# Performance work log

Measured on AMD Instinct MI355X. Metric: run time of the kernel, lower is better.

The kernel has to match this reference:

```python
import jax, jax.numpy as jnp
import numpy as np

IMG_SIZE = 256
NUM_ANGLES = 180
NUM_DETECTORS = 363
BATCH = 4


def setup_inputs() -> dict:
    key = jax.random.key(0)
    sinogram = jax.random.normal(key, (BATCH, 1, NUM_ANGLES, NUM_DETECTORS), dtype=jnp.float32)
    return {"sinogram": sinogram}


def _fbp(sinogram):
    B, C, A, D = sinogram.shape
    # --- ramp filter in frequency domain (filter_type='ramp') ---
    freq = jnp.fft.fftfreq(D).astype(jnp.float32)
    filt = jnp.abs(freq) * 2.0
    sino_fft = jnp.fft.fft(sinogram, axis=-1)
    filtered = jnp.fft.ifft(sino_fft * filt, axis=-1).real.astype(jnp.float32)  # (B,1,A,D)

    # --- backprojection (adjoint Radon), vectorized over all angles ---
    coords = jnp.linspace(-1.0, 1.0, IMG_SIZE, dtype=jnp.float32)
    y_grid, x_grid = jnp.meshgrid(coords, coords, indexing='ij')  # (H,W)
    angles = jnp.linspace(0.0, np.pi, A, dtype=jnp.float32)       # torch.linspace includes endpoint
    cos_t = jnp.cos(angles)[:, None, None]
    sin_t = jnp.sin(angles)[:, None, None]
    t = x_grid[None] * cos_t + y_grid[None] * sin_t               # (A,H,W), in [-sqrt2, sqrt2]

    # grid_sample bilinear, align_corners=True, padding_mode='zeros' along detector axis
    px = (t + 1.0) * 0.5 * (D - 1)                                # pixel coordinate
    i0 = jnp.floor(px).astype(jnp.int32)
    frac = px - i0.astype(jnp.float32)
    i1 = i0 + 1
    m0 = ((i0 >= 0) & (i0 <= D - 1)).astype(jnp.float32)
    m1 = ((i1 >= 0) & (i1 <= D - 1)).astype(jnp.float32)
    i0c = jnp.clip(i0, 0, D - 1).reshape(A, -1)                   # (A,N) N=H*W
    i1c = jnp.clip(i1, 0, D - 1).reshape(A, -1)
    w0 = ((1.0 - frac) * m0).reshape(A, -1)
    w1 = (frac * m1).reshape(A, -1)

    sino2 = filtered[:, 0]                                        # (B,A,D)
    a_idx = jnp.arange(A)[:, None]
    g0 = sino2[:, a_idx, i0c]                                     # (B,A,N)
    g1 = sino2[:, a_idx, i1c]
    recon = (g0 * w0 + g1 * w1).sum(axis=1)                       # (B,N)
    recon = recon * (np.pi / A)
    return recon.reshape(B, C, IMG_SIZE, IMG_SIZE)


def reference(sinogram):
    return _fbp(sinogram)
```

## Files before the change

kernel.cpp:

```cpp
#include <hip/hip_runtime.h>
#include <math.h>

#define D_   363
#define A_   180
#define B_   4
#define IMG_ 256

__global__ __launch_bounds__(384)
void fbp_filter(const float* __restrict__ sino,
                float* __restrict__ filtered) {
    __shared__ __align__(16) float  srow[364];
    __shared__ float                hval[D_];
    __shared__ __align__(16) float4 hext4[2 * D_];
    const int r   = blockIdx.x;
    const int tid = threadIdx.x;

    if (tid < D_) {
        srow[tid] = sino[r * D_ + tid];
        float hn;
        if (tid == 0) {
            hn = 65884.0f / 131769.0f;
        } else {
            int p1 = (181 * tid) % D_;
            int p2 = (182 * tid) % D_;
            float c1 = cosf(6.28318530717958647692f * ((float)p1 * (1.0f / 363.0f)));
            float c2 = cosf(6.28318530717958647692f * ((float)p2 * (1.0f / 363.0f)));
            float sh = sinf(3.14159265358979323846f * ((float)tid * (1.0f / 363.0f)));
            float S  = (182.0f * c1 - 181.0f * c2 - 1.0f) / (4.0f * sh * sh);
            hn = S * (4.0f / 131769.0f);
        }
        hval[tid] = hn;
    }
    if (tid == D_) srow[D_] = 0.0f;
    __syncthreads();

    for (int j = tid; j < 2 * D_; j += 384) {
        float a = hval[ j            % D_];
        float b = hval[(j + D_ - 1)  % D_];
        float c = hval[(j + D_ - 2)  % D_];
        float d = hval[(j + D_ - 3)  % D_];
        hext4[j] = make_float4(a, b, c, d);
    }
    __syncthreads();

    if (tid < D_) {
        float acc = 0.0f;
        #pragma unroll 7
        for (int q = 0; q < 91; ++q) {
            float4 sv = *(const float4*)&srow[4 * q];
            float4 hv = hext4[tid + D_ - 4 * q];
            acc = fmaf(sv.x, hv.x, acc);
            acc = fmaf(sv.y, hv.y, acc);
            acc = fmaf(sv.z, hv.z, acc);
            acc = fmaf(sv.w, hv.w, acc);
        }
        filtered[r * D_ + tid] = acc;
    }
}

__global__ __launch_bounds__(256)
void fbp_backproj(const float* __restrict__ filtered,
                  float* __restrict__ out) {
    __shared__ float cl[A_], sl[A_];
    const int tid = threadIdx.x;
    if (tid < A_) {
        float a = (float)((double)tid * (3.14159265358979323846 / 179.0));
        float sn, cn;
        sincosf(a, &sn, &cn);
        cl[tid] = 181.0f * cn;
        sl[tid] = 181.0f * sn;
    }
    __syncthreads();

    const int tile = blockIdx.x & 255;
    const int b    = blockIdx.x >> 8;
    const int ty   = tid >> 4, tx = tid & 15;
    const int i = ((tile >> 4) << 4) + ty;
    const int j = ((tile & 15) << 4) + tx;

    const float y = -1.0f + 2.0f * (float)i / 255.0f;
    const float x = -1.0f + 2.0f * (float)j / 255.0f;

    const float* __restrict__ fb = filtered + b * (A_ * D_);
    float acc = 0.0f;

    #pragma unroll 4
    for (int a = 0; a < A_; ++a) {
        float px = fmaf(x, cl[a], fmaf(y, sl[a], 181.0f));
        float fi = floorf(px);
        float frac = px - fi;
        int i0 = (int)fi;
        int i1 = i0 + 1;
        float w0 = ((unsigned)i0 <= (unsigned)(D_ - 1)) ? (1.0f - frac) : 0.0f;
        float w1 = ((unsigned)i1 <= (unsigned)(D_ - 1)) ? frac          : 0.0f;
        int i0c = min(max(i0, 0), D_ - 1);
        int i1c = min(max(i1, 0), D_ - 1);
        const float* row = fb + a * D_;
        acc = fmaf(row[i0c], w0, acc);
        acc = fmaf(row[i1c], w1, acc);
    }
    out[(b << 16) + i * IMG_ + j] = acc * (float)(M_PI / 180.0);
}

extern "C" void kernel_launch(void* const* d_in, const int* in_sizes, int n_in,
                              void* d_out, int out_size, void* d_ws, size_t ws_size,
                              hipStream_t stream) {
    const float* sino = (const float*)d_in[0];
    float* out = (float*)d_out;
    float* filtered = (float*)d_ws;

    fbp_filter  <<<B_ * A_,   384, 0, stream>>>(sino, filtered);
    fbp_backproj<<<B_ * IMG_, 256, 0, stream>>>(filtered, out);
}
```

Baseline: 92.16 us.

## Stage per-tile detector windows in shared memory for backprojection

For each 16x16 pixel tile, the backprojection kernel now computes the minimum detector index each angle can reach and loads a 36-sample window per angle into LDS. The inner loop then reads from LDS instead of doing scattered global gathers. This trades roughly 26KB of LDS per block, which may lower occupancy, plus an upfront cooperative load, for cheaper and more local reads. The window is sized on the assumption that a tile's projected footprint never exceeds 36 samples.

Measured after the change: 85.53 us. 7.2% less time.

```diff
diff --git a/kernel.cpp b/kernel.cpp
--- a/kernel.cpp
+++ b/kernel.cpp
@@ -5,6 +5,7 @@
 #define A_   180
 #define B_   4
 #define IMG_ 256
+#define W_   36
 
 __global__ __launch_bounds__(384)
 void fbp_filter(const float* __restrict__ sino,
@@ -61,43 +62,62 @@
 __global__ __launch_bounds__(256)
 void fbp_backproj(const float* __restrict__ filtered,
                   float* __restrict__ out) {
-    __shared__ float cl[A_], sl[A_];
-    const int tid = threadIdx.x;
+    __shared__ float4 csb[A_];
+    __shared__ float  win[A_ * W_];
+    const int tid  = threadIdx.x;
+    const int tile = blockIdx.x & 255;
+    const int b    = blockIdx.x >> 8;
+    const int ty   = tid >> 4, tx = tid & 15;
+    const int r0   = ((tile >> 4) << 4);
+    const int c0   = ((tile & 15) << 4);
+    const int i = r0 + ty;
+    const int j = c0 + tx;
+
     if (tid < A_) {
         float a = (float)((double)tid * (3.14159265358979323846 / 179.0));
         float sn, cn;
         sincosf(a, &sn, &cn);
-        cl[tid] = 181.0f * cn;
-        sl[tid] = 181.0f * sn;
+        float C = 181.0f * cn, S = 181.0f * sn;
+        float xa = -1.0f + 2.0f * (float)c0        / 255.0f;
+        float xb = -1.0f + 2.0f * (float)(c0 + 15) / 255.0f;
+        float ya = -1.0f + 2.0f * (float)r0        / 255.0f;
+        float yb = -1.0f + 2.0f * (float)(r0 + 15) / 255.0f;
+        float p00 = fmaf(xa, C, fmaf(ya, S, 181.0f));
+        float p01 = fmaf(xb, C, fmaf(ya, S, 181.0f));
+        float p10 = fmaf(xa, C, fmaf(yb, S, 181.0f));
+        float p11 = fmaf(xb, C, fmaf(yb, S, 181.0f));
+        float pmin = fminf(fminf(p00, p01), fminf(p10, p11));
+        csb[tid] = make_float4(C, S, floorf(pmin), 0.0f);
     }
     __syncthreads();
 
-    const int tile = blockIdx.x & 255;
-    const int b    = blockIdx.x >> 8;
-    const int ty   = tid >> 4, tx = tid & 15;
-    const int i = ((tile >> 4) << 4) + ty;
-    const int j = ((tile & 15) << 4) + tx;
+    const float* __restrict__ fb = filtered + b * (A_ * D_);
+    for (int u = tid; u < A_ * W_; u += 256) {
+        int a   = u / W_;
+        int w   = u - a * W_;
+        int idx = (int)csb[a].z + w;
+        idx = min(max(idx, 0), D_ - 1);
+        win[u] = fb[a * D_ + idx];
+    }
+    __syncthreads();
 
     const float y = -1.0f + 2.0f * (float)i / 255.0f;
     const float x = -1.0f + 2.0f * (float)j / 255.0f;
-
-    const float* __restrict__ fb = filtered + b * (A_ * D_);
     float acc = 0.0f;
 
     #pragma unroll 4
     for (int a = 0; a < A_; ++a) {
-        float px = fmaf(x, cl[a], fmaf(y, sl[a], 181.0f));
+        float4 cb = csb[a];
+        float px = fmaf(x, cb.x, fmaf(y, cb.y, 181.0f));
         float fi = floorf(px);
         float frac = px - fi;
         int i0 = (int)fi;
-        int i1 = i0 + 1;
-        float w0 = ((unsigned)i0 <= (unsigned)(D_ - 1)) ? (1.0f - frac) : 0.0f;
-        float w1 = ((unsigned)i1 <= (unsigned)(D_ - 1)) ? frac          : 0.0f;
-        int i0c = min(max(i0, 0), D_ - 1);
-        int i1c = min(max(i1, 0), D_ - 1);
-        const float* row = fb + a * D_;
-        acc = fmaf(row[i0c], w0, acc);
-        acc = fmaf(row[i1c], w1, acc);
+        int idx = i0 - (int)cb.z;
+        float w0 = ((unsigned)i0       <= (unsigned)(D_ - 1)) ? (1.0f - frac) : 0.0f;
+        float w1 = ((unsigned)(i0 + 1) <= (unsigned)(D_ - 1)) ? frac          : 0.0f;
+        const float* wrow = &win[a * W_];
+        acc = fmaf(wrow[idx],     w0, acc);
+        acc = fmaf(wrow[idx + 1], w1, acc);
     }
     out[(b << 16) + i * IMG_ + j] = acc * (float)(M_PI / 180.0);
 }
```
